# Kernel tuning notes

Hardware: AMD Instinct MI355X
Metric: run time of the kernel (lower is better)

The kernel has to match this reference:

```python
import jax, jax.numpy as jnp
import numpy as np

B, P, K = 8, 2048, 20
FEAT, POS = 3, 3
IN = FEAT + POS  # 6
OUT = 13


def _mlp2(e, wa, ba, wb, bb):
    # PyG MLP([2d,64,64]): Linear -> BatchNorm (identity at init / eval running stats) -> ReLU -> Linear (plain last)
    return jnp.maximum(e @ wa + ba, 0.0) @ wb + bb


def _edge_conv(x, wa, ba, wb, bb):
    # DynamicEdgeConv: kNN graph in current feature space (includes self like torch_cluster.knn),
    # edge feature [x_i, x_j - x_i], MLP, then max aggregation over neighbors.
    # x: [B,P,d]
    x2 = jnp.sum(x * x, axis=-1)  # [B,P]
    d2 = x2[:, :, None] + x2[:, None, :] - 2.0 * jnp.einsum('bpd,bqd->bpq', x, x)  # [B,P,P]
    idx = jax.lax.top_k(-d2, K)[1]  # [B,P,K] nearest neighbors (self included)
    xj = jax.vmap(lambda xc, ic: xc[ic])(x, idx)  # [B,P,K,d] gather
    xi = jnp.broadcast_to(x[:, :, None, :], xj.shape)
    e = jnp.concatenate([xi, xj - xi], axis=-1)  # [B,P,K,2d]
    return jnp.max(_mlp2(e, wa, ba, wb, bb), axis=2)  # [B,P,64]


def setup_inputs() -> dict:
    key = jax.random.key(0)
    ks = jax.random.split(key, 12)
    w = lambda k, s: jax.random.normal(k, s, jnp.float32) * 0.1
    z = lambda n: jnp.zeros((n,), jnp.float32)
    return {
        'feats': jax.random.normal(ks[0], (B * P, FEAT), jnp.float32),
        'pos': jax.random.normal(ks[1], (B * P, POS), jnp.float32),
        'batch': jnp.repeat(jnp.arange(B, dtype=jnp.int32), P),
        'w1a': w(ks[2], (2 * IN, 64)), 'b1a': z(64), 'w1b': w(ks[3], (64, 64)), 'b1b': z(64),
        'w2a': w(ks[4], (128, 64)), 'b2a': z(64), 'w2b': w(ks[5], (64, 64)), 'b2b': z(64),
        'w3a': w(ks[6], (128, 64)), 'b3a': z(64), 'w3b': w(ks[7], (64, 64)), 'b3b': z(64),
        'hw1': w(ks[8], (192, 1024)), 'hb1': z(1024),
        'hw2': w(ks[9], (1024, 256)), 'hb2': z(256),
        'hw3': w(ks[10], (256, 128)), 'hb3': z(128),
        'hw4': w(ks[11], (128, OUT)), 'hb4': z(OUT),
    }


def reference(feats, pos, batch, w1a, b1a, w1b, b1b, w2a, b2a, w2b, b2b,
              w3a, b3a, w3b, b3b, hw1, hb1, hw2, hb2, hw3, hb3, hw4, hb4):
    # batch is contiguous equal-size clouds -> reshape to [B,P,*]
    x0 = jnp.concatenate([feats, pos], axis=-1).reshape(B, P, IN)
    x1 = _edge_conv(x0, w1a, b1a, w1b, b1b)
    x2 = _edge_conv(x1, w2a, b2a, w2b, b2b)
    x3 = _edge_conv(x2, w3a, b3a, w3b, b3b)
    h = jnp.concatenate([x1, x2, x3], axis=-1).reshape(B * P, 192)
    # head MLP (dropout=0.5 inactive in eval, norm=None)
    h = jnp.maximum(h @ hw1 + hb1, 0.0)
    h = jnp.maximum(h @ hw2 + hb2, 0.0)
    h = jnp.maximum(h @ hw3 + hb3, 0.0)
    h = h @ hw4 + hb4
    return jax.nn.log_softmax(h, axis=1)
```

## Files before the change

kernel.cpp:

```cpp
#include <hip/hip_runtime.h>
#include <math.h>

#define BATCH 8
#define PTS   2048
#define NPTS  (BATCH * PTS)
#define KNN   20

typedef short short4v __attribute__((ext_vector_type(4)));
typedef short short8v __attribute__((ext_vector_type(8)));
typedef _Float16 half8v __attribute__((ext_vector_type(8)));
typedef float f32x4 __attribute__((ext_vector_type(4)));

__device__ __forceinline__ short f2h(float f) {
    _Float16 h = (_Float16)f;
    return __builtin_bit_cast(short, h);
}
__device__ __forceinline__ float h2f(_Float16 h) { return (float)h; }

__global__ void build_x0_kernel(const float* __restrict__ feats,
                                const float* __restrict__ pos,
                                float* __restrict__ x0) {
    int i = blockIdx.x * 256 + threadIdx.x;
    if (i >= NPTS) return;
    float* o = x0 + (size_t)i * 6;
    const float* f = feats + (size_t)i * 3;
    const float* p = pos + (size_t)i * 3;
    o[0] = f[0]; o[1] = f[1]; o[2] = f[2];
    o[3] = p[0]; o[4] = p[1]; o[5] = p[2];
}

template <int D>
__global__ void norm2_kernel(const float* __restrict__ x, float* __restrict__ xn) {
    int i = blockIdx.x * 256 + threadIdx.x;
    if (i >= NPTS) return;
    const float* r = x + (size_t)i * D;
    float s = 0.f;
#pragma unroll
    for (int j = 0; j < D; ++j) s += r[j] * r[j];
    xn[i] = s;
}

__global__ void split16_kernel(const float* __restrict__ x, unsigned short* __restrict__ xh,
                               unsigned short* __restrict__ xl) {
    int i = blockIdx.x * 256 + threadIdx.x;
    float4 v = ((const float4*)x)[i];
    float vv[4] = {v.x, v.y, v.z, v.w};
    short4v hh, ll;
#pragma unroll
    for (int j = 0; j < 4; ++j) {
        _Float16 hf = (_Float16)vv[j];
        hh[j] = __builtin_bit_cast(short, hf);
        _Float16 lf = (_Float16)(vv[j] - (float)hf);
        ll[j] = __builtin_bit_cast(short, lf);
    }
    ((short4v*)xh)[i] = hh;
    ((short4v*)xl)[i] = ll;
}

template <int D>
__global__ void __launch_bounds__(256) dist_kernel(const float* __restrict__ x,
                                                   const float* __restrict__ xn,
                                                   float* __restrict__ d2, int b0) {
    int bz = blockIdx.z;
    int b  = b0 + bz;
    const float* xb  = x  + (size_t)b * PTS * D;
    const float* xnb = xn + (size_t)b * PTS;
    float* d2b = d2 + (size_t)bz * PTS * PTS;

    __shared__ float As[64][D + 1];
    __shared__ float Bs[64][D + 1];
    int row0 = blockIdx.y * 64;
    int col0 = blockIdx.x * 64;
    int tid = threadIdx.x;
    for (int i = tid; i < 64 * D; i += 256) {
        int r = i / D, c = i - r * D;
        As[r][c] = xb[(size_t)(row0 + r) * D + c];
        Bs[r][c] = xb[(size_t)(col0 + r) * D + c];
    }
    __syncthreads();
    int tx = tid & 15, ty = tid >> 4;
    float acc[4][4] = {};
    for (int k = 0; k < D; ++k) {
        float av[4], bv[4];
#pragma unroll
        for (int i = 0; i < 4; ++i) av[i] = As[ty * 4 + i][k];
#pragma unroll
        for (int j = 0; j < 4; ++j) bv[j] = Bs[tx * 4 + j][k];
#pragma unroll
        for (int i = 0; i < 4; ++i)
#pragma unroll
            for (int j = 0; j < 4; ++j) acc[i][j] += av[i] * bv[j];
    }
#pragma unroll
    for (int i = 0; i < 4; ++i) {
        int r = row0 + ty * 4 + i;
#pragma unroll
        for (int j = 0; j < 4; ++j) {
            int c = col0 + tx * 4 + j;
            d2b[(size_t)r * PTS + c] = xnb[c] - 2.f * acc[i][j];
        }
    }
}

__global__ void __launch_bounds__(256) dist_mfma_kernel(
    const unsigned short* __restrict__ xh, const unsigned short* __restrict__ xl,
    const float* __restrict__ xn, float* __restrict__ d2, int b0)
{
    __shared__ char smem[128 * 256 + 64 * 256];
    __shared__ float sxn[64];
    char* sA = smem;
    char* sB = smem + 128 * 256;
    float* sS = (float*)smem;
    int bz = blockIdx.z, b = b0 + bz;
    int row0 = blockIdx.y * 128, col0 = blockIdx.x * 64;
    const unsigned short* xhb = xh + (size_t)b * PTS * 64;
    const unsigned short* xlb = xl + (size_t)b * PTS * 64;
    const float* xnb = xn + (size_t)b * PTS;
    float* d2b = d2 + (size_t)bz * PTS * PTS;
    int tid = threadIdx.x;

    for (int i = tid; i < 2048; i += 256) {
        int r = i >> 4, c = i & 15;
        const unsigned short* src = (c < 8) ? xhb + (size_t)(row0 + r) * 64 + (c << 3)
                                            : xlb + (size_t)(row0 + r) * 64 + ((c - 8) << 3);
        *(short8v*)(sA + ((r * 256 + (c << 4)) ^ ((r & 7) << 4))) = *(const short8v*)src;
    }
    for (int i = tid; i < 1024; i += 256) {
        int r = i >> 4, c = i & 15;
        const unsigned short* src = (c < 8) ? xhb + (size_t)(col0 + r) * 64 + (c << 3)
                                            : xlb + (size_t)(col0 + r) * 64 + ((c - 8) << 3);
        *(short8v*)(sB + ((r * 256 + (c << 4)) ^ ((r & 7) << 4))) = *(const short8v*)src;
    }
    if (tid < 64) sxn[tid] = xnb[col0 + tid];
    __syncthreads();

    int w = tid >> 6, l = tid & 63;
    int lr = l & 15, lg = l >> 4;

    half8v bh[4][2], bl[4][2];
#pragma unroll
    for (int n = 0; n < 4; ++n) {
        int c = n * 16 + lr, sw = (c & 7) << 4, base = c * 256;
#pragma unroll
        for (int ks = 0; ks < 2; ++ks) {
            bh[n][ks] = __builtin_bit_cast(half8v, *(short8v*)(sB + ((base + ks * 64 + lg * 16) ^ sw)));
            bl[n][ks] = __builtin_bit_cast(half8v, *(short8v*)(sB + ((base + 128 + ks * 64 + lg * 16) ^ sw)));
        }
    }

    f32x4 acc[2][4];
#pragma unroll
    for (int m = 0; m < 2; ++m)
#pragma unroll
        for (int n = 0; n < 4; ++n) acc[m][n] = (f32x4){0.f, 0.f, 0.f, 0.f};

#pragma unroll
    for (int m = 0; m < 2; ++m) {
        int r = w * 32 + m * 16 + lr, sw = (r & 7) << 4, base = r * 256;
        half8v ah0 = __builtin_bit_cast(half8v, *(short8v*)(sA + ((base + lg * 16) ^ sw)));
        half8v ah1 = __builtin_bit_cast(half8v, *(short8v*)(sA + ((base + 64 + lg * 16) ^ sw)));
        half8v al0 = __builtin_bit_cast(half8v, *(short8v*)(sA + ((base + 128 + lg * 16) ^ sw)));
        half8v al1 = __builtin_bit_cast(half8v, *(short8v*)(sA + ((base + 192 + lg * 16) ^ sw)));
#pragma unroll
        for (int n = 0; n < 4; ++n) {
            f32x4 a = acc[m][n];
            a = __builtin_amdgcn_mfma_f32_16x16x32_f16(ah0, bh[n][0], a, 0, 0, 0);
            a = __builtin_amdgcn_mfma_f32_16x16x32_f16(ah1, bh[n][1], a, 0, 0, 0);
            a = __builtin_amdgcn_mfma_f32_16x16x32_f16(al0, bh[n][0], a, 0, 0, 0);
            a = __builtin_amdgcn_mfma_f32_16x16x32_f16(al1, bh[n][1], a, 0, 0, 0);
            a = __builtin_amdgcn_mfma_f32_16x16x32_f16(ah0, bl[n][0], a, 0, 0, 0);
            a = __builtin_amdgcn_mfma_f32_16x16x32_f16(ah1, bl[n][1], a, 0, 0, 0);
            acc[m][n] = a;
        }
    }
    __syncthreads();

#pragma unroll
    for (int m = 0; m < 2; ++m)
#pragma unroll
        for (int n = 0; n < 4; ++n) {
            int rl = w * 32 + m * 16 + lg * 4;
            int col = n * 16 + lr;
#pragma unroll
            for (int j = 0; j < 4; ++j)
                sS[(rl + j) * 64 + col] = acc[m][n][j];
        }
    __syncthreads();

    for (int i = tid; i < 2048; i += 256) {
        int r = i >> 4, c4 = (i & 15) << 2;
        float4 v = *(float4*)&sS[r * 64 + c4];
        float4 o;
        o.x = sxn[c4 + 0] - 2.f * v.x;
        o.y = sxn[c4 + 1] - 2.f * v.y;
        o.z = sxn[c4 + 2] - 2.f * v.z;
        o.w = sxn[c4 + 3] - 2.f * v.w;
        *(float4*)&d2b[(size_t)(row0 + r) * PTS + col0 + c4] = o;
    }
}

#define GMIN8(B, GV, GJ) do {                                         \
    GV = va[(B)];     GJ = (B);                                       \
    if (va[(B)+1] < GV) { GV = va[(B)+1]; GJ = (B)+1; }               \
    if (va[(B)+2] < GV) { GV = va[(B)+2]; GJ = (B)+2; }               \
    if (va[(B)+3] < GV) { GV = va[(B)+3]; GJ = (B)+3; }               \
    if (va[(B)+4] < GV) { GV = va[(B)+4]; GJ = (B)+4; }               \
    if (va[(B)+5] < GV) { GV = va[(B)+5]; GJ = (B)+5; }               \
    if (va[(B)+6] < GV) { GV = va[(B)+6]; GJ = (B)+6; }               \
    if (va[(B)+7] < GV) { GV = va[(B)+7]; GJ = (B)+7; }               \
} while (0)

#define INVAL8(B, GV, GJ, JS) do {                                    \
    va[(B)+0] = ((B)+0 == (JS)) ? INFV : va[(B)+0];                   \
    va[(B)+1] = ((B)+1 == (JS)) ? INFV : va[(B)+1];                   \
    va[(B)+2] = ((B)+2 == (JS)) ? INFV : va[(B)+2];                   \
    va[(B)+3] = ((B)+3 == (JS)) ? INFV : va[(B)+3];                   \
    va[(B)+4] = ((B)+4 == (JS)) ? INFV : va[(B)+4];                   \
    va[(B)+5] = ((B)+5 == (JS)) ? INFV : va[(B)+5];                   \
    va[(B)+6] = ((B)+6 == (JS)) ? INFV : va[(B)+6];                   \
    va[(B)+7] = ((B)+7 == (JS)) ? INFV : va[(B)+7];                   \
    GMIN8(B, GV, GJ);                                                 \
} while (0)

__global__ void __launch_bounds__(256) topk_kernel(const float* __restrict__ d2,
                                                   int* __restrict__ nbr, int b0) {
    const float INFV = __builtin_inff();
    int wid = threadIdx.x >> 6, lane = threadIdx.x & 63;
    int pl = blockIdx.x * 4 + wid;
    int bz = blockIdx.y;
    const float* row = d2 + ((size_t)bz * PTS + pl) * PTS;

    float va[32];
#pragma unroll
    for (int j8 = 0; j8 < 8; ++j8) {
        float4 v = *(const float4*)&row[j8 * 256 + lane * 4];
        va[j8 * 4 + 0] = v.x; va[j8 * 4 + 1] = v.y;
        va[j8 * 4 + 2] = v.z; va[j8 * 4 + 3] = v.w;
    }

    float g0v, g1v, g2v, g3v;
    int   g0j, g1j, g2j, g3j;
    GMIN8(0,  g0v, g0j);
    GMIN8(8,  g1v, g1j);
    GMIN8(16, g2v, g2j);
    GMIN8(24, g3v, g3j);

    int gbase = (b0 + bz) * PTS;
    int* outp = nbr + (size_t)(gbase + pl) * KNN;

    for (int k = 0; k < KNN; ++k) {
        float lv = g0v; int lj = g0j;
        if (g1v < lv) { lv = g1v; lj = g1j; }
        if (g2v < lv) { lv = g2v; lj = g2j; }
        if (g3v < lv) { lv = g3v; lj = g3j; }
        float wm = lv;
#pragma unroll
        for (int off = 1; off < 64; off <<= 1) wm = fminf(wm, __shfl_xor(wm, off));
        int mycol = (lv == wm) ? (((lj >> 2) << 8) | (lane << 2) | (lj & 3)) : 0x7fffffff;
        int wc = mycol;
#pragma unroll
        for (int off = 1; off < 64; off <<= 1) {
            int oc = __shfl_xor(wc, off);
            wc = oc < wc ? oc : wc;
        }
        if (lane == 0) outp[k] = gbase + wc;
        if (mycol == wc) {
            int js = lj;
            int gs = js >> 3;
            if (gs == 0)      INVAL8(0,  g0v, g0j, js);
            else if (gs == 1) INVAL8(8,  g1v, g1j, js);
            else if (gs == 2) INVAL8(16, g2v, g2j, js);
            else              INVAL8(24, g3v, g3j, js);
        }
    }
}

__global__ void prep_kernel(const float* __restrict__ wa, const float* __restrict__ ba,
                            const float* __restrict__ wb,
                            float* __restrict__ wc, float* __restrict__ bc,
                            unsigned short* __restrict__ wbT, int D) {
    int t = blockIdx.x * 256 + threadIdx.x;
    if (t < D * 128) {
        int k = t >> 7, n = t & 127;
        wc[t] = (n < 64) ? (wa[k * 64 + n] - wa[(D + k) * 64 + n])
                         : wa[(D + k) * 64 + (n - 64)];
    }
    if (t < 128) bc[t] = (t < 64) ? ba[t] : 0.f;
    if (t < 4096) {
        int n = t >> 6, k = t & 63;
        wbT[t] = (unsigned short)f2h(wb[k * 64 + n]);
    }
}

__global__ void prep_head_kernel(const float* __restrict__ hw1, const float* __restrict__ hw2,
                                 const float* __restrict__ hw3,
                                 unsigned short* __restrict__ w1T, unsigned short* __restrict__ w2T,
                                 unsigned short* __restrict__ w3T) {
    int t = blockIdx.x * 256 + threadIdx.x;
    if (t < 192 * 1024) { int k = t / 1024, n = t - k * 1024; w1T[n * 192 + k] = (unsigned short)f2h(hw1[t]); }
    if (t < 1024 * 256) { int k = t >> 8, n = t & 255; w2T[n * 1024 + k] = (unsigned short)f2h(hw2[t]); }
    if (t < 256 * 128)  { int k = t >> 7, n = t & 127; w3T[n * 256 + k] = (unsigned short)f2h(hw3[t]); }
}

__global__ void uv6_kernel(const float* __restrict__ x0, const float* __restrict__ wc,
                           const float* __restrict__ bc, float* __restrict__ uvout) {
    int t = blockIdx.x * 256 + threadIdx.x;
    int i = t >> 7, n = t & 127;
    const float* xr = x0 + (size_t)i * 6;
    float s = bc[n];
#pragma unroll
    for (int r = 0; r < 6; ++r) s += xr[r] * wc[r * 128 + n];
    uvout[t] = s;
}

__global__ void __launch_bounds__(256) edge_mfma_kernel(
    const float* __restrict__ uv, const int* __restrict__ nbr,
    const unsigned short* __restrict__ wbT, const float* __restrict__ bb,
    float* __restrict__ xout, unsigned short* __restrict__ hcat16, int hoff)
{
    __shared__ short sA[256 * 64];
    __shared__ short sB[64 * 64];
    __shared__ int snbr[8 * KNN];
    char* cA = (char*)sA;
    char* cB = (char*)sB;
    int tid = threadIdx.x;
    int p0 = blockIdx.x * 8;

    if (tid < 8 * KNN) snbr[tid] = nbr[(size_t)p0 * KNN + tid];
    for (int c = tid; c < 512; c += 256) {
        int n = c >> 3, k0 = (c & 7) << 3;
        short8v w = *(const short8v*)(wbT + n * 64 + k0);
        *(short8v*)(cB + ((n * 128 + (k0 << 1)) ^ ((n & 7) << 4))) = w;
    }
    __syncthreads();

    for (int t = tid; t < 1024; t += 256) {
        int r = t >> 2, c16 = (t & 3) << 4;
        int pl = r >> 5, e = r & 31;
        short h[16] __attribute__((aligned(16)));
        if (e < KNN) {
            int q = snbr[pl * KNN + e];
            const float4* up = (const float4*)(uv + (size_t)(p0 + pl) * 128 + c16);
            const float4* vp = (const float4*)(uv + (size_t)q * 128 + 64 + c16);
#pragma unroll
            for (int j = 0; j < 4; ++j) {
                float4 uu = up[j], vv = vp[j];
                h[j * 4 + 0] = f2h(fmaxf(uu.x + vv.x, 0.f));
                h[j * 4 + 1] = f2h(fmaxf(uu.y + vv.y, 0.f));
                h[j * 4 + 2] = f2h(fmaxf(uu.z + vv.z, 0.f));
                h[j * 4 + 3] = f2h(fmaxf(uu.w + vv.w, 0.f));
            }
        } else {
#pragma unroll
            for (int j = 0; j < 16; ++j) h[j] = 0;
        }
        int base = r * 128 + (c16 << 1);
        int s = (r & 7) << 4;
        *(short8v*)(cA + (base ^ s)) = *(short8v*)(h);
        *(short8v*)(cA + ((base + 16) ^ s)) = *(short8v*)(h + 8);
    }
    __syncthreads();

    int l = tid & 63, wvv2 = tid >> 6;
    int n0 = wvv2 << 4;
    int lr = l & 15, lg = l >> 4;
    int ncol = n0 + lr;
    int sb_s = (ncol & 7) << 4;
    half8v bf0 = __builtin_bit_cast(half8v, *(short8v*)(cB + ((ncol * 128 + lg * 16) ^ sb_s)));
    half8v bf1 = __builtin_bit_cast(half8v, *(short8v*)(cB + ((ncol * 128 + 64 + lg * 16) ^ sb_s)));
    float bias = bb[ncol];

#pragma unroll
    for (int pl = 0; pl < 8; ++pl) {
        int re = (pl << 5) + lr;
        int sa_s = (re & 7) << 4;
        int rbase = re * 128;
        half8v ae0 = __builtin_bit_cast(half8v, *(short8v*)(cA + ((rbase + lg * 16) ^ sa_s)));
        half8v ae1 = __builtin_bit_cast(half8v, *(short8v*)(cA + ((rbase + 64 + lg * 16) ^ sa_s)));
        half8v ao0 = __builtin_bit_cast(half8v, *(short8v*)(cA + ((rbase + 2048 + lg * 16) ^ sa_s)));
        half8v ao1 = __builtin_bit_cast(half8v, *(short8v*)(cA + ((rbase + 2048 + 64 + lg * 16) ^ sa_s)));
        f32x4 acce = {0.f, 0.f, 0.f, 0.f};
        f32x4 acco = {0.f, 0.f, 0.f, 0.f};
        acce = __builtin_amdgcn_mfma_f32_16x16x32_f16(ae0, bf0, acce, 0, 0, 0);
        acce = __builtin_amdgcn_mfma_f32_16x16x32_f16(ae1, bf1, acce, 0, 0, 0);
        acco = __builtin_amdgcn_mfma_f32_16x16x32_f16(ao0, bf0, acco, 0, 0, 0);
        acco = __builtin_amdgcn_mfma_f32_16x16x32_f16(ao1, bf1, acco, 0, 0, 0);
        float mv = fmaxf(fmaxf(acce[0], acce[1]), fmaxf(acce[2], acce[3]));
        if (lg == 0) {
            float mo = fmaxf(fmaxf(acco[0], acco[1]), fmaxf(acco[2], acco[3]));
            mv = fmaxf(mv, mo);
        }
        mv = fmaxf(mv, __shfl_xor(mv, 16));
        mv = fmaxf(mv, __shfl_xor(mv, 32));
        if (l < 16) {
            int gp = p0 + pl;
            float o = mv + bias;
            xout[(size_t)gp * 64 + ncol] = o;
            hcat16[(size_t)gp * 192 + hoff + ncol] = (unsigned short)f2h(o);
        }
    }
}

template <int RELU>
__global__ void __launch_bounds__(256) hgemm_kernel(
    const unsigned short* __restrict__ A, const unsigned short* __restrict__ wT,
    const float* __restrict__ bias, unsigned short* __restrict__ C,
    int M, int N, int K) {
    __shared__ char sA[128 * 128];
    __shared__ char sB[64 * 128];
    int tid = threadIdx.x;
    int row0 = blockIdx.y * 128, col0 = blockIdx.x * 64;
    int w = tid >> 6, l = tid & 63;
    int lr = l & 15, lg = l >> 4;

    f32x4 acc[2][4];
#pragma unroll
    for (int m = 0; m < 2; ++m)
#pragma unroll
        for (int n = 0; n < 4; ++n) acc[m][n] = (f32x4){0.f, 0.f, 0.f, 0.f};

    for (int kt = 0; kt < K; kt += 64) {
        for (int i = tid; i < 1024; i += 256) {
            int r = i >> 3, part = i & 7;
            short8v v = *(const short8v*)(A + (size_t)(row0 + r) * K + kt + part * 8);
            *(short8v*)(sA + ((r * 128 + part * 16) ^ ((r & 7) << 4))) = v;
        }
        for (int i = tid; i < 512; i += 256) {
            int r = i >> 3, part = i & 7;
            short8v v = *(const short8v*)(wT + (size_t)(col0 + r) * K + kt + part * 8);
            *(short8v*)(sB + ((r * 128 + part * 16) ^ ((r & 7) << 4))) = v;
        }
        __syncthreads();
#pragma unroll
        for (int ks = 0; ks < 2; ++ks) {
            half8v af0, af1, bf[4];
            {
                int r = w * 32 + lr;
                af0 = __builtin_bit_cast(half8v, *(short8v*)(sA + ((r * 128 + ks * 64 + lg * 16) ^ ((r & 7) << 4))));
                int r2 = r + 16;
                af1 = __builtin_bit_cast(half8v, *(short8v*)(sA + ((r2 * 128 + ks * 64 + lg * 16) ^ ((r2 & 7) << 4))));
            }
#pragma unroll
            for (int n = 0; n < 4; ++n) {
                int c = n * 16 + lr;
                bf[n] = __builtin_bit_cast(half8v, *(short8v*)(sB + ((c * 128 + ks * 64 + lg * 16) ^ ((c & 7) << 4))));
            }
#pragma unroll
            for (int n = 0; n < 4; ++n) {
                acc[0][n] = __builtin_amdgcn_mfma_f32_16x16x32_f16(af0, bf[n], acc[0][n], 0, 0, 0);
                acc[1][n] = __builtin_amdgcn_mfma_f32_16x16x32_f16(af1, bf[n], acc[1][n], 0, 0, 0);
            }
        }
        __syncthreads();
    }
#pragma unroll
    for (int m = 0; m < 2; ++m)
#pragma unroll
        for (int n = 0; n < 4; ++n) {
            int c = col0 + n * 16 + lr;
            float bj = bias[c];
#pragma unroll
            for (int j = 0; j < 4; ++j) {
                int r = row0 + w * 32 + m * 16 + lg * 4 + j;
                float v = acc[m][n][j] + bj;
                if (RELU) v = fmaxf(v, 0.f);
                C[(size_t)r * N + c] = (unsigned short)f2h(v);
            }
        }
}

template <int RELU>
__global__ void __launch_bounds__(256) gemm_kernel(
    const float* __restrict__ A, const float* __restrict__ W,
    const float* __restrict__ bias, float* __restrict__ C,
    int M, int N, int Kd) {
    __shared__ float As[64][17];
    __shared__ float Bs[16][65];
    int row0 = blockIdx.y * 64, col0 = blockIdx.x * 64;
    int tid = threadIdx.x;
    int tx = tid & 15, ty = tid >> 4;
    float acc[4][4] = {};
    for (int kt = 0; kt < Kd; kt += 16) {
        for (int i = tid; i < 1024; i += 256) {
            int m = i >> 4, k = i & 15;
            As[m][k] = A[(size_t)(row0 + m) * Kd + kt + k];
        }
        for (int i = tid; i < 1024; i += 256) {
            int k = i >> 6, n = i & 63;
            Bs[k][n] = W[(size_t)(kt + k) * N + col0 + n];
        }
        __syncthreads();
#pragma unroll
        for (int k = 0; k < 16; ++k) {
            float av[4], bv[4];
#pragma unroll
            for (int i = 0; i < 4; ++i) av[i] = As[ty * 4 + i][k];
#pragma unroll
            for (int j = 0; j < 4; ++j) bv[j] = Bs[k][tx * 4 + j];
#pragma unroll
            for (int i = 0; i < 4; ++i)
#pragma unroll
                for (int j = 0; j < 4; ++j) acc[i][j] += av[i] * bv[j];
        }
        __syncthreads();
    }
#pragma unroll
    for (int j = 0; j < 4; ++j) {
        int c = col0 + tx * 4 + j;
        float bj = bias[c];
#pragma unroll
        for (int i = 0; i < 4; ++i) {
            int r = row0 + ty * 4 + i;
            float vv = acc[i][j] + bj;
            if (RELU) vv = fmaxf(vv, 0.f);
            C[(size_t)r * N + c] = vv;
        }
    }
}

__global__ void __launch_bounds__(256) final_kernel(const unsigned short* __restrict__ h3,
                                                    const float* __restrict__ w,
                                                    const float* __restrict__ bias,
                                                    float* __restrict__ out, int M) {
    __shared__ float sw[128 * 13];
    __shared__ float sb[13];
    int tid = threadIdx.x;
    for (int i = tid; i < 128 * 13; i += 256) sw[i] = w[i];
    if (tid < 13) sb[tid] = bias[tid];
    __syncthreads();
    int m = blockIdx.x * 256 + tid;
    if (m >= M) return;
    const short8v* hrow = (const short8v*)(h3 + (size_t)m * 128);
    float o[13];
#pragma unroll
    for (int c = 0; c < 13; ++c) o[c] = sb[c];
    for (int k8 = 0; k8 < 16; ++k8) {
        half8v hv = __builtin_bit_cast(half8v, hrow[k8]);
        int k = k8 * 8;
#pragma unroll
        for (int j = 0; j < 8; ++j) {
            float hf = h2f(hv[j]);
#pragma unroll
            for (int c = 0; c < 13; ++c) o[c] += hf * sw[(k + j) * 13 + c];
        }
    }
    float mx = o[0];
#pragma unroll
    for (int c = 1; c < 13; ++c) mx = fmaxf(mx, o[c]);
    float s = 0.f;
#pragma unroll
    for (int c = 0; c < 13; ++c) s += expf(o[c] - mx);
    float ls = logf(s);
    float* op = out + (size_t)m * 13;
#pragma unroll
    for (int c = 0; c < 13; ++c) op[c] = o[c] - mx - ls;
}

extern "C" void kernel_launch(void* const* d_in, const int* in_sizes, int n_in,
                              void* d_out, int out_size, void* d_ws, size_t ws_size,
                              hipStream_t stream) {
    const float* feats = (const float*)d_in[0];
    const float* pos   = (const float*)d_in[1];
    const float* w1a = (const float*)d_in[3];
    const float* b1a = (const float*)d_in[4];
    const float* w1b = (const float*)d_in[5];
    const float* b1b = (const float*)d_in[6];
    const float* w2a = (const float*)d_in[7];
    const float* b2a = (const float*)d_in[8];
    const float* w2b = (const float*)d_in[9];
    const float* b2b = (const float*)d_in[10];
    const float* w3a = (const float*)d_in[11];
    const float* b3a = (const float*)d_in[12];
    const float* w3b = (const float*)d_in[13];
    const float* b3b = (const float*)d_in[14];
    const float* hw1 = (const float*)d_in[15];
    const float* hb1 = (const float*)d_in[16];
    const float* hw2 = (const float*)d_in[17];
    const float* hb2 = (const float*)d_in[18];
    const float* hw3 = (const float*)d_in[19];
    const float* hb3 = (const float*)d_in[20];
    const float* hw4 = (const float*)d_in[21];
    const float* hb4 = (const float*)d_in[22];
    float* out = (float*)d_out;
    char* ws = (char*)d_ws;

    constexpr size_t OFF_X0  = 0;
    constexpr size_t OFF_X1  = OFF_X0 + (size_t)NPTS * 6 * 4;
    constexpr size_t OFF_X2  = OFF_X1 + (size_t)NPTS * 64 * 4;
    constexpr size_t OFF_X3  = OFF_X2 + (size_t)NPTS * 64 * 4;
    constexpr size_t OFF_H16 = OFF_X3 + (size_t)NPTS * 64 * 4;
    constexpr size_t OFF_IDX = OFF_H16 + (size_t)NPTS * 192 * 2;
    constexpr size_t OFF_XN  = OFF_IDX + (size_t)NPTS * KNN * 4;
    constexpr size_t OFF_WC  = OFF_XN + (size_t)NPTS * 4;
    constexpr size_t OFF_BC  = OFF_WC + 64 * 128 * 4;
    constexpr size_t OFF_WBT = OFF_BC + 128 * 4;
    constexpr size_t OFF_W1T = OFF_WBT + 4096 * 2;
    constexpr size_t OFF_W2T = OFF_W1T + (size_t)1024 * 192 * 2;
    constexpr size_t OFF_W3T = OFF_W2T + (size_t)256 * 1024 * 2;
    constexpr size_t OFF_XH  = OFF_W3T + (size_t)128 * 256 * 2;
    constexpr size_t OFF_XL  = OFF_XH + (size_t)NPTS * 64 * 2;
    constexpr size_t OFF_BIG = OFF_XL + (size_t)NPTS * 64 * 2;

    float* x0   = (float*)(ws + OFF_X0);
    float* x1   = (float*)(ws + OFF_X1);
    float* x2b  = (float*)(ws + OFF_X2);
    float* x3   = (float*)(ws + OFF_X3);
    unsigned short* hcat16 = (unsigned short*)(ws + OFF_H16);
    int*   idxb = (int*)(ws + OFF_IDX);
    float* xn   = (float*)(ws + OFF_XN);
    float* wc   = (float*)(ws + OFF_WC);
    float* bc   = (float*)(ws + OFF_BC);
    unsigned short* wbT = (unsigned short*)(ws + OFF_WBT);
    unsigned short* w1T = (unsigned short*)(ws + OFF_W1T);
    unsigned short* w2T = (unsigned short*)(ws + OFF_W2T);
    unsigned short* w3T = (unsigned short*)(ws + OFF_W3T);
    unsigned short* xh  = (unsigned short*)(ws + OFF_XH);
    unsigned short* xl  = (unsigned short*)(ws + OFF_XL);
    float* big  = (float*)(ws + OFF_BIG);
    float* uvb  = big;

    size_t avail = (ws_size > OFF_BIG) ? ws_size - OFF_BIG : 0;
    int NB = (int)(avail / ((size_t)PTS * PTS * 4));
    if (NB < 1) NB = 1;
    if (NB > 4) NB = 4;

    build_x0_kernel<<<NPTS / 256, 256, 0, stream>>>(feats, pos, x0);
    prep_head_kernel<<<1024, 256, 0, stream>>>(hw1, hw2, hw3, w1T, w2T, w3T);

    norm2_kernel<6><<<NPTS / 256, 256, 0, stream>>>(x0, xn);
    for (int b0 = 0; b0 < BATCH; b0 += NB) {
        int nb = BATCH - b0 < NB ? BATCH - b0 : NB;
        dist_kernel<6><<<dim3(PTS / 64, PTS / 64, nb), 256, 0, stream>>>(x0, xn, big, b0);
        topk_kernel<<<dim3(PTS / 4, nb), 256, 0, stream>>>(big, idxb, b0);
    }
    prep_kernel<<<32, 256, 0, stream>>>(w1a, b1a, w1b, wc, bc, wbT, 6);
    uv6_kernel<<<NPTS * 128 / 256, 256, 0, stream>>>(x0, wc, bc, uvb);
    edge_mfma_kernel<<<NPTS / 8, 256, 0, stream>>>(uvb, idxb, wbT, b1b, x1, hcat16, 0);

#define KNN64_PASS(XCUR)                                                                   \
    do {                                                                                   \
        norm2_kernel<64><<<NPTS / 256, 256, 0, stream>>>(XCUR, xn);                        \
        split16_kernel<<<NPTS * 64 / 4 / 256, 256, 0, stream>>>(XCUR, xh, xl);             \
        for (int b0 = 0; b0 < BATCH; b0 += NB) {                                           \
            int nb = BATCH - b0 < NB ? BATCH - b0 : NB;                                    \
            dist_mfma_kernel<<<dim3(PTS / 64, PTS / 128, nb), 256, 0, stream>>>(           \
                xh, xl, xn, big, b0);                                                      \
            topk_kernel<<<dim3(PTS / 4, nb), 256, 0, stream>>>(big, idxb, b0);             \
        }                                                                                  \
    } while (0)

    KNN64_PASS(x1);
    prep_kernel<<<32, 256, 0, stream>>>(w2a, b2a, w2b, wc, bc, wbT, 64);
    gemm_kernel<0><<<dim3(2, 256), 256, 0, stream>>>(x1, wc, bc, uvb, NPTS, 128, 64);
    edge_mfma_kernel<<<NPTS / 8, 256, 0, stream>>>(uvb, idxb, wbT, b2b, x2b, hcat16, 64);

    KNN64_PASS(x2b);
    prep_kernel<<<32, 256, 0, stream>>>(w3a, b3a, w3b, wc, bc, wbT, 64);
    gemm_kernel<0><<<dim3(2, 256), 256, 0, stream>>>(x2b, wc, bc, uvb, NPTS, 128, 64);
    edge_mfma_kernel<<<NPTS / 8, 256, 0, stream>>>(uvb, idxb, wbT, b3b, x3, hcat16, 128);

    size_t need = (size_t)NPTS * (1024 + 256 + 128) * 2;
    int RCH = (avail >= need) ? NPTS : 2048;
    unsigned short* h1 = (unsigned short*)big;
    unsigned short* h2 = h1 + (size_t)RCH * 1024;
    unsigned short* h3 = h2 + (size_t)RCH * 256;
    for (int c0 = 0; c0 < NPTS; c0 += RCH) {
        const unsigned short* Ain = hcat16 + (size_t)c0 * 192;
        hgemm_kernel<1><<<dim3(1024 / 64, RCH / 128), 256, 0, stream>>>(Ain, w1T, hb1, h1, RCH, 1024, 192);
        hgemm_kernel<1><<<dim3(256 / 64, RCH / 128), 256, 0, stream>>>(h1, w2T, hb2, h2, RCH, 256, 1024);
        hgemm_kernel<1><<<dim3(128 / 64, RCH / 128), 256, 0, stream>>>(h2, w3T, hb3, h3, RCH, 128, 256);
        final_kernel<<<RCH / 256, 256, 0, stream>>>(h3, hw4, hb4, out + (size_t)c0 * 13, RCH);
    }
#undef KNN64_PASS
}
```

Before: 558.9 us.

## Retile head fp16 GEMMs to 64-row by wide-column tiles with column-split waves

The head-MLP half-precision GEMM kernel now takes a compile-time column-tile width. Each block covers 64 rows and 256 or 128 columns, and the four waves split the columns instead of the rows, so each wave issues 4xNF MFMAs per k-step. For the 1024-to-256 and 256-to-128 layers one block spans the full output width, so the A tile is loaded once per row block rather than once per column block. The trade is more B-tile LDS traffic and more accumulator registers per wave, which may lower occupancy.

```diff
diff --git a/kernel.cpp b/kernel.cpp
--- a/kernel.cpp
+++ b/kernel.cpp
@@ -401,31 +401,33 @@
     }
 }
 
-template <int RELU>
+template <int RELU, int NT>
 __global__ void __launch_bounds__(256) hgemm_kernel(
     const unsigned short* __restrict__ A, const unsigned short* __restrict__ wT,
     const float* __restrict__ bias, unsigned short* __restrict__ C,
     int M, int N, int K) {
-    __shared__ char sA[128 * 128];
-    __shared__ char sB[64 * 128];
+    __shared__ char sA[64 * 128];
+    __shared__ char sB[NT * 128];
+    constexpr int NF = NT / 64;
     int tid = threadIdx.x;
-    int row0 = blockIdx.y * 128, col0 = blockIdx.x * 64;
+    int row0 = blockIdx.y * 64, col0 = blockIdx.x * NT;
     int w = tid >> 6, l = tid & 63;
     int lr = l & 15, lg = l >> 4;
-
-    f32x4 acc[2][4];
-#pragma unroll
-    for (int m = 0; m < 2; ++m)
-#pragma unroll
-        for (int n = 0; n < 4; ++n) acc[m][n] = (f32x4){0.f, 0.f, 0.f, 0.f};
+    int wcol = w * (NT / 4);
+
+    f32x4 acc[4][NF];
+#pragma unroll
+    for (int m = 0; m < 4; ++m)
+#pragma unroll
+        for (int n = 0; n < NF; ++n) acc[m][n] = (f32x4){0.f, 0.f, 0.f, 0.f};
 
     for (int kt = 0; kt < K; kt += 64) {
-        for (int i = tid; i < 1024; i += 256) {
+        for (int i = tid; i < 512; i += 256) {
             int r = i >> 3, part = i & 7;
             short8v v = *(const short8v*)(A + (size_t)(row0 + r) * K + kt + part * 8);
             *(short8v*)(sA + ((r * 128 + part * 16) ^ ((r & 7) << 4))) = v;
         }
-        for (int i = tid; i < 512; i += 256) {
+        for (int i = tid; i < NT * 8; i += 256) {
             int r = i >> 3, part = i & 7;
             short8v v = *(const short8v*)(wT + (size_t)(col0 + r) * K + kt + part * 8);
             *(short8v*)(sB + ((r * 128 + part * 16) ^ ((r & 7) << 4))) = v;
@@ -433,35 +435,34 @@
         __syncthreads();
 #pragma unroll
         for (int ks = 0; ks < 2; ++ks) {
-            half8v af0, af1, bf[4];
-            {
-                int r = w * 32 + lr;
-                af0 = __builtin_bit_cast(half8v, *(short8v*)(sA + ((r * 128 + ks * 64 + lg * 16) ^ ((r & 7) << 4))));
-                int r2 = r + 16;
-                af1 = __builtin_bit_cast(half8v, *(short8v*)(sA + ((r2 * 128 + ks * 64 + lg * 16) ^ ((r2 & 7) << 4))));
+            half8v af[4], bf[NF];
+#pragma unroll
+            for (int m = 0; m < 4; ++m) {
+                int r = m * 16 + lr;
+                af[m] = __builtin_bit_cast(half8v, *(short8v*)(sA + ((r * 128 + ks * 64 + lg * 16) ^ ((r & 7) << 4))));
             }
 #pragma unroll
-            for (int n = 0; n < 4; ++n) {
-                int c = n * 16 + lr;
+            for (int n = 0; n < NF; ++n) {
+                int c = wcol + n * 16 + lr;
                 bf[n] = __builtin_bit_cast(half8v, *(short8v*)(sB + ((c * 128 + ks * 64 + lg * 16) ^ ((c & 7) << 4))));
             }
 #pragma unroll
-            for (int n = 0; n < 4; ++n) {
-                acc[0][n] = __builtin_amdgcn_mfma_f32_16x16x32_f16(af0, bf[n], acc[0][n], 0, 0, 0);
-                acc[1][n] = __builtin_amdgcn_mfma_f32_16x16x32_f16(af1, bf[n], acc[1][n], 0, 0, 0);
-            }
+            for (int n = 0; n < NF; ++n)
+#pragma unroll
+                for (int m = 0; m < 4; ++m)
+                    acc[m][n] = __builtin_amdgcn_mfma_f32_16x16x32_f16(af[m], bf[n], acc[m][n], 0, 0, 0);
         }
         __syncthreads();
     }
 #pragma unroll
-    for (int m = 0; m < 2; ++m)
-#pragma unroll
-        for (int n = 0; n < 4; ++n) {
-            int c = col0 + n * 16 + lr;
+    for (int m = 0; m < 4; ++m)
+#pragma unroll
+        for (int n = 0; n < NF; ++n) {
+            int c = col0 + wcol + n * 16 + lr;
             float bj = bias[c];
 #pragma unroll
             for (int j = 0; j < 4; ++j) {
-                int r = row0 + w * 32 + m * 16 + lg * 4 + j;
+                int r = row0 + m * 16 + lg * 4 + j;
                 float v = acc[m][n][j] + bj;
                 if (RELU) v = fmaxf(v, 0.f);
                 C[(size_t)r * N + c] = (unsigned short)f2h(v);
@@ -666,9 +667,9 @@
     unsigned short* h3 = h2 + (size_t)RCH * 256;
     for (int c0 = 0; c0 < NPTS; c0 += RCH) {
         const unsigned short* Ain = hcat16 + (size_t)c0 * 192;
-        hgemm_kernel<1><<<dim3(1024 / 64, RCH / 128), 256, 0, stream>>>(Ain, w1T, hb1, h1, RCH, 1024, 192);
-        hgemm_kernel<1><<<dim3(256 / 64, RCH / 128), 256, 0, stream>>>(h1, w2T, hb2, h2, RCH, 256, 1024);
-        hgemm_kernel<1><<<dim3(128 / 64, RCH / 128), 256, 0, stream>>>(h2, w3T, hb3, h3, RCH, 128, 256);
+        hgemm_kernel<1, 256><<<dim3(1024 / 256, RCH / 64), 256, 0, stream>>>(Ain, w1T, hb1, h1, RCH, 1024, 192);
+        hgemm_kernel<1, 256><<<dim3(1, RCH / 64), 256, 0, stream>>>(h1, w2T, hb2, h2, RCH, 256, 1024);
+        hgemm_kernel<1, 128><<<dim3(1, RCH / 64), 256, 0, stream>>>(h2, w3T, hb3, h3, RCH, 128, 256);
         final_kernel<<<RCH / 256, 256, 0, stream>>>(h3, hw4, hb4, out + (size_t)c0 * 13, RCH);
     }
 #undef KNN64_PASS
```

New measurement: 589.8 us. 5.5% more time.
